# Performance work log

Measured on AMD Instinct MI355X. Metric: run time of the kernel, lower is better.

The kernel has to match this reference:

```python
import jax, jax.numpy as jnp
import numpy as np

BATCH = 8192
N_FEATURES = 512
DEPTH = 10
N_LEAVES = 2 ** DEPTH
ATOMS = N_FEATURES + 1  # include_one=True
TAU = 1.0


def eml(a, b):
    # Assumed definition of the custom binary eml op: smooth-max / log-sum-exp.
    # eml(a, b) = log(exp(a) + exp(b)), computed stably.
    return jnp.logaddexp(a, b)


def setup_inputs() -> dict:
    key = jax.random.key(0)
    k1, k2 = jax.random.split(key)
    X = jax.random.normal(k1, (BATCH, N_FEATURES), dtype=jnp.float32)
    leaf_logits = jax.random.normal(k2, (N_LEAVES, ATOMS), dtype=jnp.float32) * 0.1
    return {"X": X, "leaf_logits": leaf_logits}


def reference(X, leaf_logits):
    batch = X.shape[0]
    # atom values: prepend constant 1 (include_one=True) -> (batch, atoms)
    atom_values = jnp.concatenate([jnp.ones((batch, 1), dtype=X.dtype), X], axis=1)
    # softmax over atoms per leaf, then mix: (batch, n_leaves)
    weights = jax.nn.softmax(leaf_logits / TAU, axis=-1)
    current = jnp.einsum('ba,la->bl', atom_values, weights)
    # binary tree reduction: log2(n_leaves) steps over strided slices
    while current.shape[-1] > 1:
        current = eml(current[..., 0::2], current[..., 1::2])
    return current.squeeze(-1)  # (batch,)
```

## Files before the change

kernel.cpp:

```cpp
#include <hip/hip_runtime.h>
#include <hip/hip_bf16.h>

#define BATCH 8192
#define NF 512
#define NL 1024
#define ATOMS 513

typedef float float4v __attribute__((ext_vector_type(4)));
typedef short short8 __attribute__((ext_vector_type(8)));

__device__ __forceinline__ unsigned short f2bf(float f) {
    union { float f; unsigned int u; } cv; cv.f = f;
    unsigned int u = cv.u;
    u += 0x7fffu + ((u >> 16) & 1u);
    return (unsigned short)(u >> 16);
}

__device__ __forceinline__ void load_lds16(const unsigned short* g, unsigned short* ldsbase) {
    __builtin_amdgcn_global_load_lds(
        (const __attribute__((address_space(1))) unsigned int*)g,
        (__attribute__((address_space(3))) unsigned int*)ldsbase,
        16, 0, 0);
}

__global__ void convert_kernel(const float* __restrict__ X,
                               unsigned short* __restrict__ Xb) {
    size_t i = ((size_t)blockIdx.x * 256 + threadIdx.x) * 8;
    float4v x0 = *reinterpret_cast<const float4v*>(X + i);
    float4v x1 = *reinterpret_cast<const float4v*>(X + i + 4);
    short8 a;
    a[0] = (short)f2bf(x0[0]); a[1] = (short)f2bf(x0[1]);
    a[2] = (short)f2bf(x0[2]); a[3] = (short)f2bf(x0[3]);
    a[4] = (short)f2bf(x1[0]); a[5] = (short)f2bf(x1[1]);
    a[6] = (short)f2bf(x1[2]); a[7] = (short)f2bf(x1[3]);
    *reinterpret_cast<short8*>(Xb + i) = a;
}

__global__ void softmax_kernel(const float* __restrict__ logits,
                               unsigned short* __restrict__ Wb,
                               float* __restrict__ bias) {
    int l = blockIdx.x;
    int t = threadIdx.x;
    int wave = t >> 6, lane = t & 63;
    const float* row = logits + (size_t)l * ATOMS;
    float v0 = row[t];
    float v1 = row[t + 256];
    float v2 = (t == 0) ? row[512] : -1e30f;

    __shared__ float red[8];
    float m = fmaxf(fmaxf(v0, v1), v2);
#pragma unroll
    for (int o = 32; o > 0; o >>= 1) m = fmaxf(m, __shfl_xor(m, o, 64));
    if (lane == 0) red[wave] = m;
    __syncthreads();
    float mx = fmaxf(fmaxf(red[0], red[1]), fmaxf(red[2], red[3]));

    float e0 = __expf(v0 - mx);
    float e1 = __expf(v1 - mx);
    float e2 = (t == 0) ? __expf(v2 - mx) : 0.f;
    float s = e0 + e1 + e2;
#pragma unroll
    for (int o = 32; o > 0; o >>= 1) s += __shfl_xor(s, o, 64);
    if (lane == 0) red[4 + wave] = s;
    __syncthreads();
    float inv = 1.f / (red[4] + red[5] + red[6] + red[7]);

    unsigned short* wrow = Wb + (size_t)l * NF;
    if (t == 0) {
        bias[l] = e0 * inv;
        wrow[511] = f2bf(e2 * inv);
    } else {
        wrow[t - 1] = f2bf(e0 * inv);
    }
    wrow[t + 255] = f2bf(e1 * inv);
}

__global__ __launch_bounds__(256, 2)
void gemm_lse_kernel(const unsigned short* __restrict__ Xb,
                     const unsigned short* __restrict__ Wb,
                     const float* __restrict__ bias,
                     float* __restrict__ partial) {
    __shared__ unsigned short As[2][128 * 32];
    __shared__ unsigned short Bs[2][128 * 32];
    __shared__ float sums[2][128];

    int tid  = threadIdx.x;
    int wave = tid >> 6;
    int lane = tid & 63;
    int quad = lane >> 4;
    int l16  = lane & 15;
    int wr = wave >> 1;
    int wc = wave & 1;

    int mb = blockIdx.x >> 3;
    int nb = blockIdx.x & 7;
    int R0 = mb * 128;
    int N0 = nb * 128;

    int srow  = wave * 32 + (lane >> 2);
    int selem = (lane & 3) * 8;
    const unsigned short* ga = Xb + (size_t)(R0 + srow) * NF + selem;
    const unsigned short* gb = Wb + (size_t)(N0 + srow) * NF + selem;

    float4v acc[4][4];
#pragma unroll
    for (int mt = 0; mt < 4; ++mt)
#pragma unroll
        for (int nt = 0; nt < 4; ++nt)
            acc[mt][nt] = (float4v){0.f, 0.f, 0.f, 0.f};

    {
        load_lds16(ga,           &As[0][(wave * 32) * 32]);
        load_lds16(ga + 16 * NF, &As[0][(wave * 32 + 16) * 32]);
        load_lds16(gb,           &Bs[0][(wave * 32) * 32]);
        load_lds16(gb + 16 * NF, &Bs[0][(wave * 32 + 16) * 32]);
    }
    __syncthreads();

    int frag_off = (wr * 64 + l16) * 32 + quad * 8;

    for (int kt = 0; kt < 16; ++kt) {
        int cur = kt & 1;
        if (kt < 15) {
            const unsigned short* a = ga + (kt + 1) * 32;
            const unsigned short* b = gb + (kt + 1) * 32;
            int nxt = cur ^ 1;
            load_lds16(a,           &As[nxt][(wave * 32) * 32]);
            load_lds16(a + 16 * NF, &As[nxt][(wave * 32 + 16) * 32]);
            load_lds16(b,           &Bs[nxt][(wave * 32) * 32]);
            load_lds16(b + 16 * NF, &Bs[nxt][(wave * 32 + 16) * 32]);
        }

        short8 af[4], bfr[4];
#pragma unroll
        for (int mt = 0; mt < 4; ++mt)
            af[mt] = *reinterpret_cast<const short8*>(
                &As[cur][frag_off + (mt * 16 - wr * 64 + wr * 64) * 32 + (mt * 0)]);
#pragma unroll
        for (int mt = 0; mt < 4; ++mt)
            af[mt] = *reinterpret_cast<const short8*>(
                &As[cur][(wr * 64 + mt * 16 + l16) * 32 + quad * 8]);
#pragma unroll
        for (int nt = 0; nt < 4; ++nt)
            bfr[nt] = *reinterpret_cast<const short8*>(
                &Bs[cur][(wc * 64 + nt * 16 + l16) * 32 + quad * 8]);

#pragma unroll
        for (int mt = 0; mt < 4; ++mt)
#pragma unroll
            for (int nt = 0; nt < 4; ++nt)
                acc[mt][nt] = __builtin_amdgcn_mfma_f32_16x16x32_bf16(
                    af[mt], bfr[nt], acc[mt][nt], 0, 0, 0);

        __syncthreads();
    }

    float bl[4];
#pragma unroll
    for (int nt = 0; nt < 4; ++nt)
        bl[nt] = bias[N0 + wc * 64 + nt * 16 + l16];

    float ps[4][4];
#pragma unroll
    for (int mt = 0; mt < 4; ++mt)
#pragma unroll
        for (int r = 0; r < 4; ++r) ps[mt][r] = 0.f;

#pragma unroll
    for (int nt = 0; nt < 4; ++nt)
#pragma unroll
        for (int mt = 0; mt < 4; ++mt)
#pragma unroll
            for (int r = 0; r < 4; ++r)
                ps[mt][r] += __expf(acc[mt][nt][r] + bl[nt]);

#pragma unroll
    for (int m = 1; m < 16; m <<= 1)
#pragma unroll
        for (int mt = 0; mt < 4; ++mt)
#pragma unroll
            for (int r = 0; r < 4; ++r)
                ps[mt][r] += __shfl_xor(ps[mt][r], m, 64);

    if (l16 == 0) {
#pragma unroll
        for (int mt = 0; mt < 4; ++mt)
#pragma unroll
            for (int r = 0; r < 4; ++r)
                sums[wc][wr * 64 + mt * 16 + quad * 4 + r] = ps[mt][r];
    }
    __syncthreads();
    if (tid < 128)
        partial[(size_t)nb * BATCH + R0 + tid] = sums[0][tid] + sums[1][tid];
}

__global__ void combine_kernel(const float* __restrict__ partial,
                               float* __restrict__ out) {
    int i = blockIdx.x * 256 + threadIdx.x;
    float s = 0.f;
#pragma unroll
    for (int c = 0; c < 8; ++c) s += partial[(size_t)c * BATCH + i];
    out[i] = logf(s);
}

extern "C" void kernel_launch(void* const* d_in, const int* in_sizes, int n_in,
                              void* d_out, int out_size, void* d_ws, size_t ws_size,
                              hipStream_t stream) {
    const float* X      = (const float*)d_in[0];
    const float* logits = (const float*)d_in[1];
    float* out = (float*)d_out;

    char* ws = (char*)d_ws;
    unsigned short* Xb   = (unsigned short*)ws;
    unsigned short* Wb   = (unsigned short*)(ws + (size_t)BATCH * NF * 2);
    float* bias = (float*)(ws + (size_t)BATCH * NF * 2 + (size_t)NL * NF * 2);
    float* part = (float*)((char*)bias + NL * sizeof(float));

    convert_kernel<<<(BATCH * NF) / (256 * 8), 256, 0, stream>>>(X, Xb);
    softmax_kernel<<<NL, 256, 0, stream>>>(logits, Wb, bias);
    gemm_lse_kernel<<<(BATCH / 128) * (NL / 128), 256, 0, stream>>>(Xb, Wb, bias, part);
    combine_kernel<<<BATCH / 256, 256, 0, stream>>>(part, out);
}
```

Before: 84.84 us.

## Give each wave private LDS tiles and replace block barriers with vmcnt waits

Each wave now loads its own 64-row A and B slices into a private double-buffered LDS region, so the per-iteration __syncthreads is removed and waves wait only on their own outstanding global-to-LDS loads via s_waitcnt vmcnt. This removes cross-wave barrier stalls but duplicates global loads: each A and B row block is now fetched by two waves, doubling global/L2 traffic and LDS usage (64KB vs 32KB), which may reduce occupancy. Correctness relies on the hand-coded waitcnt encodings and on LDS-DMA completion being covered by vmcnt without an explicit barrier.

```diff
diff --git a/kernel.cpp b/kernel.cpp
--- a/kernel.cpp
+++ b/kernel.cpp
@@ -22,6 +22,9 @@
         (__attribute__((address_space(3))) unsigned int*)ldsbase,
         16, 0, 0);
 }
+
+#define WAIT_VMCNT_8() __builtin_amdgcn_s_waitcnt(0x0F78)
+#define WAIT_VMCNT_0() __builtin_amdgcn_s_waitcnt(0x0F70)
 
 __global__ void convert_kernel(const float* __restrict__ X,
                                unsigned short* __restrict__ Xb) {
@@ -80,8 +83,7 @@
                      const unsigned short* __restrict__ Wb,
                      const float* __restrict__ bias,
                      float* __restrict__ partial) {
-    __shared__ unsigned short As[2][128 * 32];
-    __shared__ unsigned short Bs[2][128 * 32];
+    __shared__ unsigned short lds[4][2][4096];
     __shared__ float sums[2][128];
 
     int tid  = threadIdx.x;
@@ -97,10 +99,10 @@
     int R0 = mb * 128;
     int N0 = nb * 128;
 
-    int srow  = wave * 32 + (lane >> 2);
-    int selem = (lane & 3) * 8;
-    const unsigned short* ga = Xb + (size_t)(R0 + srow) * NF + selem;
-    const unsigned short* gb = Wb + (size_t)(N0 + srow) * NF + selem;
+    unsigned short* myL = &lds[wave][0][0];
+
+    const unsigned short* gA = Xb + (size_t)(R0 + wr * 64 + (lane >> 2)) * NF + (lane & 3) * 8;
+    const unsigned short* gB = Wb + (size_t)(N0 + wc * 64 + (lane >> 2)) * NF + (lane & 3) * 8;
 
     float4v acc[4][4];
 #pragma unroll
@@ -109,41 +111,36 @@
         for (int nt = 0; nt < 4; ++nt)
             acc[mt][nt] = (float4v){0.f, 0.f, 0.f, 0.f};
 
-    {
-        load_lds16(ga,           &As[0][(wave * 32) * 32]);
-        load_lds16(ga + 16 * NF, &As[0][(wave * 32 + 16) * 32]);
-        load_lds16(gb,           &Bs[0][(wave * 32) * 32]);
-        load_lds16(gb + 16 * NF, &Bs[0][(wave * 32 + 16) * 32]);
-    }
-    __syncthreads();
-
-    int frag_off = (wr * 64 + l16) * 32 + quad * 8;
+#pragma unroll
+    for (int j = 0; j < 4; ++j) {
+        load_lds16(gA + j * 16 * NF, myL + j * 512);
+        load_lds16(gB + j * 16 * NF, myL + 2048 + j * 512);
+    }
 
     for (int kt = 0; kt < 16; ++kt) {
         int cur = kt & 1;
         if (kt < 15) {
-            const unsigned short* a = ga + (kt + 1) * 32;
-            const unsigned short* b = gb + (kt + 1) * 32;
-            int nxt = cur ^ 1;
-            load_lds16(a,           &As[nxt][(wave * 32) * 32]);
-            load_lds16(a + 16 * NF, &As[nxt][(wave * 32 + 16) * 32]);
-            load_lds16(b,           &Bs[nxt][(wave * 32) * 32]);
-            load_lds16(b + 16 * NF, &Bs[nxt][(wave * 32 + 16) * 32]);
+            unsigned short* dst = myL + (cur ^ 1) * 4096;
+            const unsigned short* a = gA + (kt + 1) * 32;
+            const unsigned short* b = gB + (kt + 1) * 32;
+#pragma unroll
+            for (int j = 0; j < 4; ++j) {
+                load_lds16(a + j * 16 * NF, dst + j * 512);
+                load_lds16(b + j * 16 * NF, dst + 2048 + j * 512);
+            }
+            WAIT_VMCNT_8();
+        } else {
+            WAIT_VMCNT_0();
         }
 
+        const unsigned short* base = myL + cur * 4096;
         short8 af[4], bfr[4];
 #pragma unroll
         for (int mt = 0; mt < 4; ++mt)
-            af[mt] = *reinterpret_cast<const short8*>(
-                &As[cur][frag_off + (mt * 16 - wr * 64 + wr * 64) * 32 + (mt * 0)]);
-#pragma unroll
-        for (int mt = 0; mt < 4; ++mt)
-            af[mt] = *reinterpret_cast<const short8*>(
-                &As[cur][(wr * 64 + mt * 16 + l16) * 32 + quad * 8]);
+            af[mt] = *reinterpret_cast<const short8*>(base + (mt * 16 + l16) * 32 + quad * 8);
 #pragma unroll
         for (int nt = 0; nt < 4; ++nt)
-            bfr[nt] = *reinterpret_cast<const short8*>(
-                &Bs[cur][(wc * 64 + nt * 16 + l16) * 32 + quad * 8]);
+            bfr[nt] = *reinterpret_cast<const short8*>(base + 2048 + (nt * 16 + l16) * 32 + quad * 8);
 
 #pragma unroll
         for (int mt = 0; mt < 4; ++mt)
@@ -151,8 +148,6 @@
             for (int nt = 0; nt < 4; ++nt)
                 acc[mt][nt] = __builtin_amdgcn_mfma_f32_16x16x32_bf16(
                     af[mt], bfr[nt], acc[mt][nt], 0, 0, 0);
-
-        __syncthreads();
     }
 
     float bl[4];
```

Measured after the change: 89.59 us. 5.6% more time.
